# Performance work log

Hardware: AMD Instinct MI355X
Metric: run time of the kernel (lower is better)

## Reference

```python
import jax, jax.numpy as jnp
import numpy as np

E = 1024  # embed_dim

def setup_inputs() -> dict:
    key = jax.random.key(0)
    ks = jax.random.split(key, 7)
    s = 1.0 / np.sqrt(E)  # torch Linear default init scale (uniform bound)
    x = jax.random.normal(ks[0], (4, 2048, E), dtype=jnp.float32)
    Wq = jax.random.uniform(ks[1], (E, E), jnp.float32, -s, s)
    bq = jax.random.uniform(ks[2], (E,), jnp.float32, -s, s)
    Wk = jax.random.uniform(ks[3], (E, E), jnp.float32, -s, s)
    bk = jax.random.uniform(ks[4], (E,), jnp.float32, -s, s)
    Wv = jax.random.uniform(ks[5], (E, E), jnp.float32, -s, s)
    bv = jax.random.uniform(ks[6], (E,), jnp.float32, -s, s)
    return {"x": x, "Wq": Wq, "bq": bq, "Wk": Wk, "bk": bk, "Wv": Wv, "bv": bv}

def reference(x, Wq, bq, Wk, bk, Wv, bv):
    # torch nn.Linear: y = x @ W.T + b
    Q = jnp.einsum('bse,fe->bsf', x, Wq) + bq
    K = jnp.einsum('bse,fe->bsf', x, Wk) + bk
    V = jnp.einsum('bse,fe->bsf', x, Wv) + bv
    scale = jnp.sqrt(jnp.asarray(E, x.dtype))
    scores = jnp.einsum('bqd,bkd->bqk', Q, K) / scale  # [B,S,S]
    attn = jax.nn.softmax(scores, axis=-1)
    return jnp.einsum('bqk,bkd->bqd', attn, V)
```

## Files before the change

### kernel.cpp

```cpp
#include <hip/hip_runtime.h>
#include <hip/hip_bf16.h>


typedef __attribute__((ext_vector_type(8))) short bf16x8;
typedef __attribute__((ext_vector_type(4))) float f32x4;

#define DEVI static __device__ __forceinline__

DEVI short to_bf16(float f) {
    unsigned u = __builtin_bit_cast(unsigned, f);
    u += 0x7fffu + ((u >> 16) & 1u);
    return (short)(u >> 16);
}
DEVI float from_bf16(short s) {
    return __builtin_bit_cast(float, (unsigned)((unsigned short)s) << 16);
}

DEVI void gload_lds16(const short* g, short* l) {
    __builtin_amdgcn_global_load_lds(
        (const __attribute__((address_space(1))) void*)g,
        (__attribute__((address_space(3))) void*)l, 16, 0, 0);
}

template<int BIAS, int EPI, typename TOUT>
__global__ __launch_bounds__(256, 3)
void gemm97(const short* __restrict__ A, long lda, long bsA,
            const short* __restrict__ B, long ldb, long bsB,
            const float* __restrict__ b0, const float* __restrict__ b1,
            const float* __restrict__ b2,
            TOUT* __restrict__ c0, TOUT* __restrict__ c1, TOUT* __restrict__ c2,
            long ldc, long bsC, int K, float scale,
            const float* __restrict__ rs, long rsLD, float* __restrict__ ps)
{
    __shared__ __align__(16) short As[128 * 64];
    __shared__ __align__(16) short Bs[128 * 64];

    const int tid = threadIdx.x;
    const int z = blockIdx.z;

    const int gx = gridDim.x;
    const int nwg = gx * gridDim.y;
    const int id = blockIdx.y * gx + blockIdx.x;
    const int id2 = (id & 7) * (nwg >> 3) + (id >> 3);
    const long m0 = (long)(id2 / gx) * 128;
    const long n0 = (long)(id2 % gx) * 128;

    const short* Ab = A + (long)z * bsA + m0 * lda;
    const short* Bb = B + (long)z * bsB + n0 * ldb;

    const int wv = tid >> 6;
    const int lane = tid & 63;
    const int wr = (wv >> 1) * 64;
    const int wc = (wv & 1) * 64;
    const int lrow = lane & 15;
    const int q = lane >> 4;

    const int NT = K >> 6;

    auto stage = [&](int t) {
        const long k0 = (long)t * 64;
        #pragma unroll
        for (int i = 0; i < 4; ++i) {
            int s = i * 256 + tid;
            int row = s >> 3;
            int src = (s & 7) ^ (row & 7);
            gload_lds16(Ab + (long)row * lda + k0 + src * 8, &As[s * 8]);
        }
        #pragma unroll
        for (int i = 0; i < 4; ++i) {
            int s = i * 256 + tid;
            int row = s >> 3;
            int src = (s & 7) ^ (row & 7);
            gload_lds16(Bb + (long)row * ldb + k0 + src * 8, &Bs[s * 8]);
        }
    };

    f32x4 acc[4][4] = {};

    for (int t = 0; t < NT; ++t) {
        if (t) {
            asm volatile("s_waitcnt lgkmcnt(0)" ::: "memory");
            __builtin_amdgcn_sched_barrier(0);
            __builtin_amdgcn_s_barrier();
        }
        stage(t);
        asm volatile("s_waitcnt vmcnt(0)" ::: "memory");
        __builtin_amdgcn_sched_barrier(0);
        __builtin_amdgcn_s_barrier();

        bf16x8 af[4][2], bf[4][2];
        #pragma unroll
        for (int m = 0; m < 4; ++m) {
            int row = wr + m * 16 + lrow;
            #pragma unroll
            for (int kk = 0; kk < 2; ++kk) {
                int ch = (kk * 4 + q) ^ (row & 7);
                af[m][kk] = *(const bf16x8*)&As[row * 64 + ch * 8];
            }
        }
        #pragma unroll
        for (int n = 0; n < 4; ++n) {
            int row = wc + n * 16 + lrow;
            #pragma unroll
            for (int kk = 0; kk < 2; ++kk) {
                int ch = (kk * 4 + q) ^ (row & 7);
                bf[n][kk] = *(const bf16x8*)&Bs[row * 64 + ch * 8];
            }
        }

        __builtin_amdgcn_s_setprio(1);
        #pragma unroll
        for (int m = 0; m < 4; ++m)
            #pragma unroll
            for (int n = 0; n < 4; ++n)
                #pragma unroll
                for (int kk = 0; kk < 2; ++kk)
                    acc[m][n] = __builtin_amdgcn_mfma_f32_16x16x32_bf16(
                        af[m][kk], bf[n][kk], acc[m][n], 0, 0, 0);
        __builtin_amdgcn_s_setprio(0);
    }

    const float* bias = (BIAS == 2) ? b0
                      : ((z == 0) ? b0 : (z == 1) ? b1 : b2);
    TOUT* Cz = ((z == 0) ? c0 : (z == 1) ? c1 : c2) + (long)z * bsC;
    TOUT* Cb = Cz + m0 * ldc + n0;
    #pragma unroll
    for (int m = 0; m < 4; ++m) {
        #pragma unroll
        for (int r = 0; r < 4; ++r) {
            int row = wr + m * 16 + q * 4 + r;
            float iv = 1.0f;
            if constexpr (EPI == 2)
                iv = 1.0f / rs[(long)z * rsLD + m0 + row];
            float rsum = 0.f;
            #pragma unroll
            for (int n = 0; n < 4; ++n) {
                int col = wc + n * 16 + lrow;
                float v = acc[m][n][r] * scale;
                if constexpr (BIAS == 1) v += bias[n0 + col];
                if constexpr (BIAS == 2) v += bias[m0 + row];
                if constexpr (EPI == 1) { v = __expf(v); rsum += v; }
                if constexpr (EPI == 2) v *= iv;
                if constexpr (sizeof(TOUT) == 2)
                    Cb[(long)row * ldc + col] = to_bf16(v);
                else
                    Cb[(long)row * ldc + col] = v;
            }
            if constexpr (EPI == 1) {
                rsum += __shfl_xor(rsum, 1);
                rsum += __shfl_xor(rsum, 2);
                rsum += __shfl_xor(rsum, 4);
                rsum += __shfl_xor(rsum, 8);
                if (lrow == 0) {
                    int j = (int)(n0 >> 7) * 2 + (wc >> 6);
                    ps[((long)z * 32 + j) * 2048 + m0 + row] = rsum;
                }
            }
        }
    }
}

__global__ __launch_bounds__(256)
void cvt_all(const float* __restrict__ x,
             const float* __restrict__ wq, const float* __restrict__ wk,
             const float* __restrict__ wv, short* __restrict__ dst)
{
    const int y = blockIdx.y;
    const float* src;
    long dstOff8;
    long i;
    if (y < 8) {
        src = x;
        i = ((long)y * 512 + blockIdx.x) * 256 + threadIdx.x;
        dstOff8 = 0;
    } else {
        src = (y == 8) ? wq : (y == 9) ? wk : wv;
        i = (long)blockIdx.x * 256 + threadIdx.x;
        dstOff8 = (8l * 1024 * 1024 + (long)(y - 8) * 1024 * 1024) / 8;
    }
    float4 a = ((const float4*)src)[2 * i];
    float4 b = ((const float4*)src)[2 * i + 1];
    bf16x8 o = { to_bf16(a.x), to_bf16(a.y), to_bf16(a.z), to_bf16(a.w),
                 to_bf16(b.x), to_bf16(b.y), to_bf16(b.z), to_bf16(b.w) };
    *(bf16x8*)&dst[(dstOff8 + i) * 8] = o;
}

__global__ __launch_bounds__(256)
void reduce_rs(const float* __restrict__ ps, float* __restrict__ rs)
{
    int row = blockIdx.x * 256 + threadIdx.x;
    int z = row >> 11, r = row & 2047;
    const float* p = ps + (long)z * 32 * 2048 + r;
    float s = 0.f;
    #pragma unroll
    for (int j = 0; j < 32; ++j) s += p[j * 2048];
    rs[row] = s;
}

extern "C" void kernel_launch(void* const* d_in, const int* in_sizes, int n_in,
                              void* d_out, int out_size, void* d_ws, size_t ws_size,
                              hipStream_t stream)
{
    (void)in_sizes; (void)n_in; (void)out_size; (void)ws_size;

    const float* x  = (const float*)d_in[0];
    const float* Wq = (const float*)d_in[1];
    const float* bq = (const float*)d_in[2];
    const float* Wk = (const float*)d_in[3];
    const float* bk = (const float*)d_in[4];
    const float* Wv = (const float*)d_in[5];
    const float* bv = (const float*)d_in[6];
    float* out = (float*)d_out;

    const int S = 2048, E = 1024;
    const long M1 = 1024l * 1024;

    short* w  = (short*)d_ws;
    short* Q  = w;
    short* Kb = w + 8 * M1;
    short* P  = w + 16 * M1;
    float* rs = (float*)w;
    short* VT = w + 8 * M1;

    short* dows = (short*)d_out;
    short* xb = dows;
    short* Wb = dows + 8 * M1;
    float* psum = (float*)(dows + 11 * M1);

    dim3 blk(256);

    cvt_all<<<dim3(512, 11), blk, 0, stream>>>(x, Wq, Wk, Wv, xb);

    gemm97<1, 0, short><<<dim3(8, 64, 2), blk, 0, stream>>>(
        xb, E, 0, Wb, E, M1, bq, bk, nullptr, Q, Kb, nullptr, E, 0, E, 1.0f,
        nullptr, 0, nullptr);

    gemm97<0, 1, short><<<dim3(16, 16, 4), blk, 0, stream>>>(
        Q, E, 2 * M1, Kb, E, 2 * M1, nullptr, nullptr, nullptr,
        P, P, P, S, 4 * M1, E, 0.03125f, nullptr, 0, psum);

    gemm97<2, 0, short><<<dim3(16, 8, 4), blk, 0, stream>>>(
        Wb + 2 * M1, E, 0, xb, E, 2 * M1, bv, nullptr, nullptr,
        VT, VT, VT, S, 2 * M1, E, 1.0f, nullptr, 0, nullptr);

    reduce_rs<<<dim3(32), blk, 0, stream>>>(psum, rs);

    gemm97<0, 2, float><<<dim3(8, 16, 4), blk, 0, stream>>>(
        P, S, 4 * M1, VT, S, 2 * M1, nullptr, nullptr, nullptr,
        out, out, out, E, 2 * M1, S, 1.0f, rs, S, nullptr);
}
```

Baseline: 179.3 us.

## Add 256x256 double-buffered GEMM kernel for QK projection and score GEMMs

Adds a new 512-thread GEMM kernel with 256x256 output tiles that splits each 64-wide K step into two 32-wide halves. Global-to-LDS loads are double-buffered, so the next tile's loads overlap the MFMA work on the current one, and a new LDS swizzle is used. The kernel replaces the old 128x128 single-buffered kernel for the Q/K projection and the QK^T score GEMM, aiming for more data reuse and better latency hiding. The cost is one workgroup per CU, higher register pressure and fewer workgroups in the grid. The old kernel is also simplified by dropping its unused multi-output and row-sum paths.

```diff
diff --git a/kernel.cpp b/kernel.cpp
--- a/kernel.cpp
+++ b/kernel.cpp
@@ -22,15 +22,170 @@
         (__attribute__((address_space(3))) void*)l, 16, 0, 0);
 }
 
+#define BAR()   __builtin_amdgcn_s_barrier()
+#define LGKM0() do { asm volatile("s_waitcnt lgkmcnt(0)" ::: "memory"); \
+                     __builtin_amdgcn_sched_barrier(0); } while (0)
+
+template<int BIAS, int EPI, typename TOUT>
+__global__ __launch_bounds__(512, 1)
+void gemm256(const short* __restrict__ A, long lda, long bsA,
+             const short* __restrict__ B, long ldb, long bsB,
+             const float* __restrict__ b0, const float* __restrict__ b1,
+             const float* __restrict__ b2,
+             TOUT* __restrict__ c0, TOUT* __restrict__ c1, TOUT* __restrict__ c2,
+             long ldc, long bsC, int K, float scale, float* __restrict__ ps)
+{
+    __shared__ __align__(16) short Al[2][2][256 * 32];
+    __shared__ __align__(16) short Bl[2][2][256 * 32];
+
+    const int tid = threadIdx.x;
+    const int z = blockIdx.z;
+    const int gx = gridDim.x;
+    const int nwg = gx * gridDim.y;
+    const int id = blockIdx.y * gx + blockIdx.x;
+    const int id2 = (id & 7) * (nwg >> 3) + (id >> 3);
+    const long m0 = (long)(id2 / gx) * 256;
+    const long n0 = (long)(id2 % gx) * 256;
+
+    const short* Ab = A + (long)z * bsA + m0 * lda;
+    const short* Bb = B + (long)z * bsB + n0 * ldb;
+
+    const int wv = tid >> 6;
+    const int wm = wv >> 2;
+    const int wn = wv & 3;
+    const int lane = tid & 63;
+    const int lrow = lane & 15;
+    const int q = lane >> 4;
+
+    const int NT = K >> 6;
+
+    int srow[2], soff[2];
+    #pragma unroll
+    for (int i = 0; i < 2; ++i) {
+        int s = i * 512 + tid;
+        srow[i] = s >> 2;
+        soff[i] = ((((s & 3) - srow[i] - (srow[i] >> 2)) & 3)) * 8;
+    }
+
+    auto stA = [&](int t, int kh) {
+        const long k0 = (long)t * 64 + kh * 32;
+        short* dst = &Al[t & 1][kh][0];
+        #pragma unroll
+        for (int i = 0; i < 2; ++i)
+            gload_lds16(Ab + (long)srow[i] * lda + k0 + soff[i],
+                        &dst[(i * 512 + tid) * 8]);
+    };
+    auto stB = [&](int t, int kh) {
+        const long k0 = (long)t * 64 + kh * 32;
+        short* dst = &Bl[t & 1][kh][0];
+        #pragma unroll
+        for (int i = 0; i < 2; ++i)
+            gload_lds16(Bb + (long)srow[i] * ldb + k0 + soff[i],
+                        &dst[(i * 512 + tid) * 8]);
+    };
+
+    bf16x8 af[4], bf[4];
+    auto rdA = [&](int b, int kh, int mh) {
+        #pragma unroll
+        for (int m = 0; m < 4; ++m) {
+            int row = wm * 128 + (mh * 4 + m) * 16 + lrow;
+            int p = (q + row + (row >> 2)) & 3;
+            af[m] = *(const bf16x8*)&Al[b][kh][row * 32 + p * 8];
+        }
+    };
+    auto rdB = [&](int b, int kh) {
+        #pragma unroll
+        for (int n = 0; n < 4; ++n) {
+            int row = wn * 64 + n * 16 + lrow;
+            int p = (q + row + (row >> 2)) & 3;
+            bf[n] = *(const bf16x8*)&Bl[b][kh][row * 32 + p * 8];
+        }
+    };
+
+    f32x4 acc[8][4] = {};
+
+    auto MM = [&](int mh) {
+        __builtin_amdgcn_s_setprio(1);
+        #pragma unroll
+        for (int m = 0; m < 4; ++m)
+            #pragma unroll
+            for (int n = 0; n < 4; ++n)
+                acc[mh * 4 + m][n] = __builtin_amdgcn_mfma_f32_16x16x32_bf16(
+                    af[m], bf[n], acc[mh * 4 + m][n], 0, 0, 0);
+        __builtin_amdgcn_s_setprio(0);
+    };
+
+    stA(0, 0); stB(0, 0); stA(0, 1); stB(0, 1);
+    stA(1, 0); stB(1, 0);
+    asm volatile("s_waitcnt vmcnt(4)" ::: "memory");
+    __builtin_amdgcn_sched_barrier(0);
+    BAR();
+
+    for (int t = 0; t < NT; ++t) {
+        const int b = t & 1;
+        rdA(b, 0, 0); rdB(b, 0);
+        if (t + 1 < NT) stA(t + 1, 1);
+        BAR(); LGKM0(); MM(0); BAR();
+        rdA(b, 0, 1);
+        if (t + 1 < NT) stB(t + 1, 1);
+        BAR(); LGKM0(); MM(1);
+        if (t < NT - 1) asm volatile("s_waitcnt vmcnt(8)" ::: "memory");
+        else            asm volatile("s_waitcnt vmcnt(0)" ::: "memory");
+        __builtin_amdgcn_sched_barrier(0);
+        BAR();
+        rdA(b, 1, 0); rdB(b, 1);
+        if (t + 2 < NT) stA(t + 2, 0);
+        BAR(); LGKM0(); MM(0); BAR();
+        rdA(b, 1, 1);
+        if (t + 2 < NT) stB(t + 2, 0);
+        BAR(); LGKM0(); MM(1);
+        if (t < NT - 2) asm volatile("s_waitcnt vmcnt(8)" ::: "memory");
+        else            asm volatile("s_waitcnt vmcnt(0)" ::: "memory");
+        __builtin_amdgcn_sched_barrier(0);
+        BAR();
+    }
+
+    const float* bias = (z == 0) ? b0 : (z == 1) ? b1 : b2;
+    TOUT* Cb = (((z == 0) ? c0 : (z == 1) ? c1 : c2) + (long)z * bsC)
+               + m0 * ldc + n0;
+    #pragma unroll
+    for (int m = 0; m < 8; ++m) {
+        #pragma unroll
+        for (int r = 0; r < 4; ++r) {
+            int row = wm * 128 + m * 16 + q * 4 + r;
+            float rsum = 0.f;
+            #pragma unroll
+            for (int n = 0; n < 4; ++n) {
+                int col = wn * 64 + n * 16 + lrow;
+                float v = acc[m][n][r] * scale;
+                if constexpr (BIAS == 1) v += bias[n0 + col];
+                if constexpr (EPI == 1) { v = __expf(v); rsum += v; }
+                if constexpr (sizeof(TOUT) == 2)
+                    Cb[(long)row * ldc + col] = to_bf16(v);
+                else
+                    Cb[(long)row * ldc + col] = v;
+            }
+            if constexpr (EPI == 1) {
+                rsum += __shfl_xor(rsum, 1);
+                rsum += __shfl_xor(rsum, 2);
+                rsum += __shfl_xor(rsum, 4);
+                rsum += __shfl_xor(rsum, 8);
+                if (lrow == 0) {
+                    int j = (int)(n0 >> 6) + wn;
+                    ps[((long)z * 32 + j) * 2048 + m0 + row] = rsum;
+                }
+            }
+        }
+    }
+}
+
 template<int BIAS, int EPI, typename TOUT>
 __global__ __launch_bounds__(256, 3)
 void gemm97(const short* __restrict__ A, long lda, long bsA,
             const short* __restrict__ B, long ldb, long bsB,
-            const float* __restrict__ b0, const float* __restrict__ b1,
-            const float* __restrict__ b2,
-            TOUT* __restrict__ c0, TOUT* __restrict__ c1, TOUT* __restrict__ c2,
-            long ldc, long bsC, int K, float scale,
-            const float* __restrict__ rs, long rsLD, float* __restrict__ ps)
+            const float* __restrict__ b0,
+            TOUT* __restrict__ C, long ldc, long bsC, int K, float scale,
+            const float* __restrict__ rs, long rsLD)
 {
     __shared__ __align__(16) short As[128 * 64];
     __shared__ __align__(16) short Bs[128 * 64];
@@ -78,15 +233,11 @@
     f32x4 acc[4][4] = {};
 
     for (int t = 0; t < NT; ++t) {
-        if (t) {
-            asm volatile("s_waitcnt lgkmcnt(0)" ::: "memory");
-            __builtin_amdgcn_sched_barrier(0);
-            __builtin_amdgcn_s_barrier();
-        }
+        if (t) { LGKM0(); BAR(); }
         stage(t);
         asm volatile("s_waitcnt vmcnt(0)" ::: "memory");
         __builtin_amdgcn_sched_barrier(0);
-        __builtin_amdgcn_s_barrier();
+        BAR();
 
         bf16x8 af[4][2], bf[4][2];
         #pragma unroll
@@ -120,10 +271,7 @@
         __builtin_amdgcn_s_setprio(0);
     }
 
-    const float* bias = (BIAS == 2) ? b0
-                      : ((z == 0) ? b0 : (z == 1) ? b1 : b2);
-    TOUT* Cz = ((z == 0) ? c0 : (z == 1) ? c1 : c2) + (long)z * bsC;
-    TOUT* Cb = Cz + m0 * ldc + n0;
+    TOUT* Cb = C + (long)z * bsC + m0 * ldc + n0;
     #pragma unroll
     for (int m = 0; m < 4; ++m) {
         #pragma unroll
@@ -132,29 +280,16 @@
             float iv = 1.0f;
             if constexpr (EPI == 2)
                 iv = 1.0f / rs[(long)z * rsLD + m0 + row];
-            float rsum = 0.f;
             #pragma unroll
             for (int n = 0; n < 4; ++n) {
                 int col = wc + n * 16 + lrow;
                 float v = acc[m][n][r] * scale;
-                if constexpr (BIAS == 1) v += bias[n0 + col];
-                if constexpr (BIAS == 2) v += bias[m0 + row];
-                if constexpr (EPI == 1) { v = __expf(v); rsum += v; }
+                if constexpr (BIAS == 2) v += b0[m0 + row];
                 if constexpr (EPI == 2) v *= iv;
                 if constexpr (sizeof(TOUT) == 2)
                     Cb[(long)row * ldc + col] = to_bf16(v);
                 else
                     Cb[(long)row * ldc + col] = v;
-            }
-            if constexpr (EPI == 1) {
-                rsum += __shfl_xor(rsum, 1);
-                rsum += __shfl_xor(rsum, 2);
-                rsum += __shfl_xor(rsum, 4);
-                rsum += __shfl_xor(rsum, 8);
-                if (lrow == 0) {
-                    int j = (int)(n0 >> 7) * 2 + (wc >> 6);
-                    ps[((long)z * 32 + j) * 2048 + m0 + row] = rsum;
-                }
             }
         }
     }
@@ -227,25 +362,25 @@
     short* Wb = dows + 8 * M1;
     float* psum = (float*)(dows + 11 * M1);
 
-    dim3 blk(256);
+    dim3 blk(256), blk5(512);
 
     cvt_all<<<dim3(512, 11), blk, 0, stream>>>(x, Wq, Wk, Wv, xb);
 
-    gemm97<1, 0, short><<<dim3(8, 64, 2), blk, 0, stream>>>(
+    gemm256<1, 0, short><<<dim3(4, 32, 2), blk5, 0, stream>>>(
         xb, E, 0, Wb, E, M1, bq, bk, nullptr, Q, Kb, nullptr, E, 0, E, 1.0f,
-        nullptr, 0, nullptr);
-
-    gemm97<0, 1, short><<<dim3(16, 16, 4), blk, 0, stream>>>(
+        nullptr);
+
+    gemm256<0, 1, short><<<dim3(8, 8, 4), blk5, 0, stream>>>(
         Q, E, 2 * M1, Kb, E, 2 * M1, nullptr, nullptr, nullptr,
-        P, P, P, S, 4 * M1, E, 0.03125f, nullptr, 0, psum);
+        P, P, P, S, 4 * M1, E, 0.03125f, psum);
 
     gemm97<2, 0, short><<<dim3(16, 8, 4), blk, 0, stream>>>(
-        Wb + 2 * M1, E, 0, xb, E, 2 * M1, bv, nullptr, nullptr,
-        VT, VT, VT, S, 2 * M1, E, 1.0f, nullptr, 0, nullptr);
+        Wb + 2 * M1, E, 0, xb, E, 2 * M1, bv, VT, S, 2 * M1, E, 1.0f,
+        nullptr, 0);
 
     reduce_rs<<<dim3(32), blk, 0, stream>>>(psum, rs);
 
     gemm97<0, 2, float><<<dim3(8, 16, 4), blk, 0, stream>>>(
-        P, S, 4 * M1, VT, S, 2 * M1, nullptr, nullptr, nullptr,
-        out, out, out, E, 2 * M1, S, 1.0f, rs, S, nullptr);
-}
+        P, S, 4 * M1, VT, S, 2 * M1, nullptr, out, E, 2 * M1, S, 1.0f,
+        rs, S);
+}
```

Measured after the change: 167.6 us. -6.5%, faster.
